# Performance work log

Hardware: AMD Instinct MI355X
Metric: run time of the kernel (lower is better)

## Reference

```python
import jax, jax.numpy as jnp
import numpy as np

B, S, D, H, R, P = 4, 8192, 512, 8, 64, 4
HD = D // H  # 64
EPS = 1e-6


def _sketch_p4(z, G1, G2):
    # sketchwithnegativity(z, 2): M1 = M2 = z
    inv_sqrt_r = 1.0 / np.sqrt(R).astype(np.float32)
    half = inv_sqrt_r * ((z @ G1) * (z @ G2))  # [B,H,S,R]
    return half * half  # sketch(): half * half for p=4


def setup_inputs() -> dict:
    key = jax.random.key(0)
    ks = jax.random.split(key, 16)
    lin = lambda k: jax.random.normal(k, (D, D), jnp.float32) * (1.0 / np.sqrt(D))
    g = lambda k: jax.random.normal(k, (HD, R), jnp.float32) * (1.0 / np.sqrt(R))
    return {
        "x": jax.random.normal(ks[0], (B, S, D), jnp.float32),
        "Wq": lin(ks[1]), "bq": jnp.zeros((D,), jnp.float32),
        "Wk": lin(ks[2]), "bk": jnp.zeros((D,), jnp.float32),
        "Wv": lin(ks[3]), "bv": jnp.zeros((D,), jnp.float32),
        "Wp": lin(ks[4]), "bp": jnp.zeros((D,), jnp.float32),
        "gamma_q": jnp.ones((1,), jnp.float32), "beta_q": jnp.zeros((1,), jnp.float32),
        "gamma_k": jnp.ones((1,), jnp.float32), "beta_k": jnp.zeros((1,), jnp.float32),
        "qG1": g(ks[5]), "qG2": g(ks[6]),
        "kG1": g(ks[7]), "kG2": g(ks[8]),
    }


def reference(x, Wq, bq, Wk, bk, Wv, bv, Wp, bp,
              gamma_q, beta_q, gamma_k, beta_k, qG1, qG2, kG1, kG2):
    b, s, d = x.shape
    split = lambda t: t.reshape(b, s, H, HD).transpose(0, 2, 1, 3)  # [B,H,S,HD]
    q = split(x @ Wq + bq)
    k = split(x @ Wk + bk)
    v = split(x @ Wv + bv)
    q = gamma_q * q + beta_q
    k = gamma_k * k + beta_k
    phi_q = _sketch_p4(q, qG1, qG2)  # [B,H,S,R]
    phi_k = _sketch_p4(k, kG1, kG2)  # [B,H,S,R]
    # linear-attention form of attn = (phi_q phi_k^T) / rowsum; avoids [S,S]
    kv = jnp.einsum('bhsr,bhsd->bhrd', phi_k, v)          # [B,H,R,HD]
    ksum = phi_k.sum(axis=2)                              # [B,H,R]
    num = jnp.einsum('bhqr,bhrd->bhqd', phi_q, kv)        # [B,H,S,HD]
    den = jnp.einsum('bhqr,bhr->bhq', phi_q, ksum) + EPS  # [B,H,S]
    out = num / den[..., None]
    out = out.transpose(0, 2, 1, 3).reshape(b, s, d)
    return out @ Wp + bp
```

## Files before the change

### kernel.cpp

```cpp
#include <hip/hip_runtime.h>
#include <hip/hip_bf16.h>


#define SEQ 8192

typedef __attribute__((ext_vector_type(8))) short bf16x8;
typedef __attribute__((ext_vector_type(4))) float f32x4;

__device__ __forceinline__ unsigned short f2b(float f) {
    union { float f; unsigned int i; } v; v.f = f;
    unsigned int r = v.i + 0x7fffu + ((v.i >> 16) & 1u);
    return (unsigned short)(r >> 16);
}
__device__ __forceinline__ float b2f(unsigned short u) {
    union { unsigned int i; float f; } v; v.i = ((unsigned int)u) << 16; return v.f;
}

#if __has_builtin(__builtin_amdgcn_global_load_lds)
#define ASYNC_CP 1
#endif

__device__ __forceinline__ void cp16(const unsigned short* g, unsigned short* l) {
#ifdef ASYNC_CP
    __builtin_amdgcn_global_load_lds(
        (const __attribute__((address_space(1))) unsigned int*)g,
        (__attribute__((address_space(3))) unsigned int*)l, 16, 0, 0);
#endif
}

#define SBAR      asm volatile("s_barrier" ::: "memory")
#define WAITV(n)  asm volatile("s_waitcnt vmcnt(" #n ")" ::: "memory")

__global__ __launch_bounds__(256) void prep_all(
    const float* __restrict__ x, unsigned short* __restrict__ xb,
    const float* __restrict__ Wv, const float* __restrict__ Wp,
    unsigned short* __restrict__ WTf, unsigned short* __restrict__ WTp,
    const float* __restrict__ Wq, const float* __restrict__ bq,
    const float* __restrict__ Wk, const float* __restrict__ bk,
    const float* __restrict__ bv,
    const float* __restrict__ gq, const float* __restrict__ bbq,
    const float* __restrict__ gk, const float* __restrict__ bbk,
    const float* __restrict__ qG1, const float* __restrict__ qG2,
    const float* __restrict__ kG1, const float* __restrict__ kG2,
    float* __restrict__ cvec)
{
    const int blk = blockIdx.x;
    const int tid = threadIdx.x;

    if (blk < 8192) {
        size_t i = ((size_t)blk * 256 + tid) * 8;
        float4 a = *(const float4*)&x[i];
        float4 b = *(const float4*)&x[i + 4];
        ushort4 o1 = { f2b(a.x), f2b(a.y), f2b(a.z), f2b(a.w) };
        ushort4 o2 = { f2b(b.x), f2b(b.y), f2b(b.z), f2b(b.w) };
        *(ushort4*)&xb[i]     = o1;
        *(ushort4*)&xb[i + 4] = o2;
        return;
    }

    if (blk < 8704) {
        const int idx = blk - 8192;
        const int z = idx >> 8;
        const float* W = (z == 0) ? Wv : Wp;
        unsigned short* O = (z == 0) ? (WTf + (size_t)2048 * 512) : WTp;
        __shared__ float t[32][33];
        const int tx = tid & 31, ty = tid >> 5;
        const int k0 = ((idx >> 4) & 15) * 32, n0 = (idx & 15) * 32;
        #pragma unroll
        for (int i = 0; i < 4; ++i)
            t[ty + 8 * i][tx] = W[(size_t)(k0 + ty + 8 * i) * 512 + n0 + tx];
        __syncthreads();
        #pragma unroll
        for (int i = 0; i < 4; ++i)
            O[(size_t)(n0 + ty + 8 * i) * 512 + k0 + tx] = f2b(t[tx][ty + 8 * i]);
        return;
    }

    const int idx = blk - 8704;
    if (idx == 512) {
        for (int i = tid; i < 512; i += 256) cvec[2048 + i] = bv[i];
        return;
    }
    const int bi = idx & 31, ky = idx >> 5;
    const int zz = bi >> 4, h = (bi >> 1) & 7, p = bi & 1;
    const float* W    = zz ? Wk : Wq;
    const float* bias = zz ? bk : bq;
    const float* G    = zz ? (p ? kG2 : kG1) : (p ? qG2 : qG1);
    const float  gamma = zz ? gk[0] : gq[0];
    const float  beta  = zz ? bbk[0] : bbq[0];

    __shared__ float Gs[64][65];
    for (int i = tid; i < 4096; i += 256) Gs[i >> 6][i & 63] = G[i];
    __syncthreads();

    const int rr = tid & 63, kg = tid >> 6;
    const int jc = zz * 1024 + h * 128 + rr * 2 + p;
    const int k0 = ky * 32;
    for (int k = k0 + kg; k < k0 + 32; k += 4) {
        float s = 0.f;
        const float* wrow = &W[(size_t)k * 512 + h * 64];
        #pragma unroll 8
        for (int j = 0; j < 64; ++j) s = fmaf(wrow[j], Gs[j][rr], s);
        WTf[(size_t)jc * 512 + k] = f2b(gamma * s);
    }
    if (kg == 0 && ky == 0) {
        float cb = 0.f, cg = 0.f;
        #pragma unroll 8
        for (int j = 0; j < 64; ++j) {
            cb = fmaf(bias[h * 64 + j], Gs[j][rr], cb);
            cg += Gs[j][rr];
        }
        cvec[jc] = gamma * cb + beta * cg;
    }
}

#define STAGE_P(kk, off)                                                        \
    do {                                                                        \
        unsigned short* dA = sm + (off) + (w * 32) * 32;                        \
        cp16(gA + (kk), dA);                                                    \
        cp16(gA + 16 * 512 + (kk), dA + 16 * 32);                               \
        unsigned short* dB = sm + (off) + 4096 + (w * 32) * 32;                 \
        cp16(gB + (kk), dB);                                                    \
        cp16(gB + 16 * 512 + (kk), dB + 16 * 32);                               \
    } while (0)

#define COMPUTE_P(off)                                                          \
    do {                                                                        \
        bf16x8 af[4], bfr[4];                                                   \
        _Pragma("unroll")                                                       \
        for (int i = 0; i < 4; ++i) {                                           \
            af[i]  = *(const bf16x8*)&sm[(off) + (wr * 64 + i * 16 + (lane & 15)) * 32 + cr]; \
            bfr[i] = *(const bf16x8*)&sm[(off) + 4096 + (wc * 64 + i * 16 + (lane & 15)) * 32 + cr]; \
        }                                                                       \
        __builtin_amdgcn_s_setprio(1);                                          \
        _Pragma("unroll")                                                       \
        for (int mi = 0; mi < 4; ++mi)                                          \
            _Pragma("unroll")                                                   \
            for (int ni = 0; ni < 4; ++ni)                                      \
                acc[mi][ni] = __builtin_amdgcn_mfma_f32_16x16x32_bf16(          \
                    af[mi], bfr[ni], acc[mi][ni], 0, 0, 0);                     \
        __builtin_amdgcn_s_setprio(0);                                          \
    } while (0)

#define KLOOP_P                                                                 \
    do {                                                                        \
        STAGE_P(0, 0u);                                                         \
        STAGE_P(32, 8192u);                                                     \
        unsigned o0 = 0u, o1 = 8192u, o2 = 16384u;                              \
        _Pragma("unroll 1")                                                     \
        for (int t = 0; t < 16; ++t) {                                          \
            SBAR;                               \
            if (t < 14) {                                                       \
                STAGE_P((t + 2) * 32, o2);                                      \
                WAITV(8);                       \
            } else if (t == 14) {                                               \
                WAITV(4);                                                       \
            } else {                                                            \
                WAITV(0);                                                       \
            }                                                                   \
            SBAR;                               \
            COMPUTE_P(o0);                                                      \
            unsigned tmp = o0; o0 = o1; o1 = o2; o2 = tmp;                      \
        }                                                                       \
    } while (0)

__global__ __launch_bounds__(256) void gemm_mfma_fused(
    const unsigned short* __restrict__ xb,
    const unsigned short* __restrict__ WTf,
    const float* __restrict__ cvec,
    unsigned short* __restrict__ PHIQ, unsigned short* __restrict__ PHIKT,
    unsigned short* __restrict__ VT)
{
    __shared__ __align__(16) unsigned short smem[24576];
    unsigned short* sm = smem;

    const int tid = threadIdx.x;
    const int w = tid >> 6, lane = tid & 63;
    const int flat = blockIdx.x;
    const int xcd = flat & 7, slot = flat >> 3;
    const int n0 = (xcd * 32 + slot / 20) * 128;
    const int j0 = (slot % 20) * 128;
    const int wr = w >> 1, wc = w & 1;

    const int r0 = w * 32 + (lane >> 2);
    const int kq = (lane & 3) * 8;
    const unsigned short* gA = &xb[(size_t)(n0 + r0) * 512 + kq];
    const unsigned short* gB = &WTf[(size_t)(j0 + r0) * 512 + kq];

    f32x4 acc[4][4];
    #pragma unroll
    for (int i = 0; i < 4; ++i)
        #pragma unroll
        for (int j = 0; j < 4; ++j) { acc[i][j] = (f32x4){0.f, 0.f, 0.f, 0.f}; }

    const int cr = (lane >> 4) * 8;

    KLOOP_P;

    const int bq = n0 >> 13;
    const int sq = n0 & (SEQ - 1);
    const int t0 = sq + wr * 64 + (lane >> 4) * 4;

    if (j0 < 2048) {
        const int zq = j0 >> 10;
        const int h  = (j0 >> 7) & 7;
        #pragma unroll
        for (int ni = 0; ni < 4; ++ni) {
            const int loc = wc * 64 + ni * 16 + (lane & 15);
            const float cv = cvec[j0 + loc];
            const int rr = loc >> 1;
            #pragma unroll
            for (int mi = 0; mi < 4; ++mi) {
                float ph[4];
                #pragma unroll
                for (int r = 0; r < 4; ++r) {
                    float u = acc[mi][ni][r] + cv;
                    float up = __shfl_xor(u, 1);
                    float hh = 0.125f * u * up;
                    ph[r] = hh * hh;
                }
                if ((lane & 1) == 0) {
                    if (zq == 0) {
                        #pragma unroll
                        for (int r = 0; r < 4; ++r)
                            PHIQ[((size_t)(bq * 8 + h) * SEQ + t0 + mi * 16 + r) * 64 + rr]
                                = f2b(ph[r]);
                    } else {
                        ushort4 o = { f2b(ph[0]), f2b(ph[1]), f2b(ph[2]), f2b(ph[3]) };
                        *(ushort4*)&PHIKT[((size_t)((bq * 8 + h) * 64 + rr)) * SEQ
                                          + t0 + mi * 16] = o;
                    }
                }
            }
        }
    } else {
        #pragma unroll
        for (int ni = 0; ni < 4; ++ni) {
            const int loc = wc * 64 + ni * 16 + (lane & 15);
            const int n = (j0 - 2048) + loc;
            const float cv = cvec[j0 + loc];
            #pragma unroll
            for (int mi = 0; mi < 4; ++mi) {
                ushort4 o = { f2b(acc[mi][ni][0] + cv), f2b(acc[mi][ni][1] + cv),
                              f2b(acc[mi][ni][2] + cv), f2b(acc[mi][ni][3] + cv) };
                *(ushort4*)&VT[((size_t)(bq * 512 + n)) * SEQ + t0 + mi * 16] = o;
            }
        }
    }
}

__global__ __launch_bounds__(256) void gemm_mfma_final(
    const unsigned short* __restrict__ Ab,
    const unsigned short* __restrict__ WTp,
    const float* __restrict__ bias, float* __restrict__ out)
{
    __shared__ __align__(16) unsigned short smem[24576];
    unsigned short* sm = smem;

    const int tid = threadIdx.x;
    const int w = tid >> 6, lane = tid & 63;
    const int flat = blockIdx.x;
    const int xcd = flat & 7, slot = flat >> 3;
    const int n0 = (xcd * 32 + (slot >> 2)) * 128;
    const int j0 = (slot & 3) * 128;
    const int wr = w >> 1, wc = w & 1;

    const int r0 = w * 32 + (lane >> 2);
    const int kq = (lane & 3) * 8;
    const unsigned short* gA = &Ab[(size_t)(n0 + r0) * 512 + kq];
    const unsigned short* gB = &WTp[(size_t)(j0 + r0) * 512 + kq];

    f32x4 acc[4][4];
    #pragma unroll
    for (int i = 0; i < 4; ++i)
        #pragma unroll
        for (int j = 0; j < 4; ++j) { acc[i][j] = (f32x4){0.f, 0.f, 0.f, 0.f}; }

    const int cr = (lane >> 4) * 8;

    KLOOP_P;

    #pragma unroll
    for (int ni = 0; ni < 4; ++ni) {
        const int jcol = j0 + wc * 64 + ni * 16 + (lane & 15);
        const float bvv = bias[jcol];
        #pragma unroll
        for (int mi = 0; mi < 4; ++mi) {
            #pragma unroll
            for (int r = 0; r < 4; ++r) {
                const int t = n0 + wr * 64 + mi * 16 + (lane >> 4) * 4 + r;
                out[(size_t)t * 512 + jcol] = acc[mi][ni][r] + bvv;
            }
        }
    }
}

__global__ __launch_bounds__(256) void kv_mfma(
    const unsigned short* __restrict__ PHIKT, const unsigned short* __restrict__ VT,
    float* __restrict__ KVP, float* __restrict__ KSP)
{
    const int bh = blockIdx.x, seg = blockIdx.y;
    const int tid = threadIdx.x;
    const int w = tid >> 6, lane = tid & 63;
    const size_t pbase =
        ((size_t)bh * 64 + w * 16 + (lane & 15)) * SEQ + seg * 256 + (lane >> 4) * 8;
    const size_t vbase =
        ((size_t)((bh >> 3) * 512 + (bh & 7) * 64 + (lane & 15))) * SEQ
        + seg * 256 + (lane >> 4) * 8;

    f32x4 acc[4], ks;
    #pragma unroll
    for (int nt = 0; nt < 4; ++nt) acc[nt] = (f32x4){0.f, 0.f, 0.f, 0.f};
    ks = (f32x4){0.f, 0.f, 0.f, 0.f};
    bf16x8 ones;
    #pragma unroll
    for (int i = 0; i < 8; ++i) ones[i] = (short)0x3f80;

    #pragma unroll 2
    for (int k = 0; k < 256; k += 32) {
        bf16x8 a = *(const bf16x8*)&PHIKT[pbase + k];
        ks = __builtin_amdgcn_mfma_f32_16x16x32_bf16(a, ones, ks, 0, 0, 0);
        #pragma unroll
        for (int nt = 0; nt < 4; ++nt) {
            bf16x8 bb = *(const bf16x8*)&VT[vbase + (size_t)nt * 16 * SEQ + k];
            acc[nt] = __builtin_amdgcn_mfma_f32_16x16x32_bf16(a, bb, acc[nt], 0, 0, 0);
        }
    }

    float* kvp = &KVP[((size_t)bh * 32 + seg) * 4096];
    #pragma unroll
    for (int nt = 0; nt < 4; ++nt) {
        float4 o = { acc[nt][0], acc[nt][1], acc[nt][2], acc[nt][3] };
        *(float4*)&kvp[(nt * 16 + (lane & 15)) * 64 + w * 16 + (lane >> 4) * 4] = o;
    }
    if ((lane & 15) == 0) {
        float4 o = { ks[0], ks[1], ks[2], ks[3] };
        *(float4*)&KSP[((size_t)bh * 32 + seg) * 64 + w * 16 + (lane >> 4) * 4] = o;
    }
}

__global__ __launch_bounds__(256) void kv_reduce(
    const float* __restrict__ KVP, const float* __restrict__ KSP,
    float* __restrict__ KV, float* __restrict__ KS)
{
    const int bh = blockIdx.x;
    const int e0 = blockIdx.y * 512;
    for (int e = e0 + threadIdx.x; e < e0 + 512; e += 256) {
        float s = 0.f;
        #pragma unroll 8
        for (int c = 0; c < 32; ++c) s += KVP[(size_t)(bh * 32 + c) * 4096 + e];
        KV[(size_t)bh * 4096 + e] = s;
    }
    if (blockIdx.y == 0 && threadIdx.x < 64) {
        float s = 0.f;
        for (int c = 0; c < 32; ++c) s += KSP[(bh * 32 + c) * 64 + threadIdx.x];
        KS[bh * 64 + threadIdx.x] = s;
    }
}

__global__ __launch_bounds__(256) void attn_mfma(
    const unsigned short* __restrict__ PHIQ, const float* __restrict__ KV,
    const float* __restrict__ KS, unsigned short* __restrict__ OAb)
{
    __shared__ __align__(16) unsigned short bpad[144 * 72];
    const int bh = blockIdx.x, st = blockIdx.y;
    const int tid = threadIdx.x;
    const int b = bh >> 3, h = bh & 7;

    for (int i = tid; i < 144 * 64; i += 256) {
        const int n = i >> 6, r = i & 63;
        float val;
        if (n < 64)        val = KV[(size_t)bh * 4096 + n * 64 + r];
        else if (n < 128)  { float x = KV[(size_t)bh * 4096 + (n - 64) * 64 + r];
                             val = x - b2f(f2b(x)); }
        else if (n == 128) val = KS[bh * 64 + r];
        else if (n == 129) { float x = KS[bh * 64 + r]; val = x - b2f(f2b(x)); }
        else               val = 0.f;
        bpad[n * 72 + r] = f2b(val);
    }
    __syncthreads();

    const int w = tid >> 6, lane = tid & 63;
    bf16x8 bf[9][2];
    #pragma unroll
    for (int nt = 0; nt < 9; ++nt) {
        const unsigned short* bp = &bpad[(nt * 16 + (lane & 15)) * 72 + (lane >> 4) * 8];
        bf[nt][0] = *(const bf16x8*)bp;
        bf[nt][1] = *(const bf16x8*)(bp + 32);
    }

    const int tw = st * 256 + w * 64;
    #pragma unroll
    for (int mt = 0; mt < 4; ++mt) {
        const unsigned short* ap =
            &PHIQ[((size_t)bh * SEQ + tw + mt * 16 + (lane & 15)) * 64 + (lane >> 4) * 8];
        bf16x8 a0 = *(const bf16x8*)ap;
        bf16x8 a1 = *(const bf16x8*)(ap + 32);
        f32x4 acc[9];
        #pragma unroll
        for (int nt = 0; nt < 9; ++nt) acc[nt] = (f32x4){0.f, 0.f, 0.f, 0.f};
        #pragma unroll
        for (int nt = 0; nt < 9; ++nt) {
            acc[nt] = __builtin_amdgcn_mfma_f32_16x16x32_bf16(a0, bf[nt][0], acc[nt], 0, 0, 0);
            acc[nt] = __builtin_amdgcn_mfma_f32_16x16x32_bf16(a1, bf[nt][1], acc[nt], 0, 0, 0);
        }
        #pragma unroll
        for (int r4 = 0; r4 < 4; ++r4) {
            const float den = __shfl(acc[8][r4], (lane & 48)) +
                              __shfl(acc[8][r4], (lane & 48) + 1) + 1e-6f;
            const float inv = 1.0f / den;
            const int s = tw + mt * 16 + (lane >> 4) * 4 + r4;
            #pragma unroll
            for (int nt = 0; nt < 4; ++nt)
                OAb[((size_t)b * SEQ + s) * 512 + h * 64 + nt * 16 + (lane & 15)] =
                    f2b((acc[nt][r4] + acc[nt + 4][r4]) * inv);
        }
    }
}

extern "C" void kernel_launch(void* const* d_in, const int* in_sizes, int n_in,
                              void* d_out, int out_size, void* d_ws, size_t ws_size,
                              hipStream_t stream)
{
    (void)in_sizes; (void)n_in; (void)out_size; (void)ws_size;
    const float* x   = (const float*)d_in[0];
    const float* Wq  = (const float*)d_in[1];
    const float* bq  = (const float*)d_in[2];
    const float* Wk  = (const float*)d_in[3];
    const float* bk  = (const float*)d_in[4];
    const float* Wv  = (const float*)d_in[5];
    const float* bv  = (const float*)d_in[6];
    const float* Wp  = (const float*)d_in[7];
    const float* bp  = (const float*)d_in[8];
    const float* gq  = (const float*)d_in[9];
    const float* bbq = (const float*)d_in[10];
    const float* gk  = (const float*)d_in[11];
    const float* bbk = (const float*)d_in[12];
    const float* qG1 = (const float*)d_in[13];
    const float* qG2 = (const float*)d_in[14];
    const float* kG1 = (const float*)d_in[15];
    const float* kG2 = (const float*)d_in[16];

    unsigned short* PHIQ  = (unsigned short*)d_ws;
    unsigned short* PHIKT = PHIQ + 16777216;
    unsigned short* VT    = PHIKT + 16777216;
    unsigned short* xb    = VT   + 16777216;
    unsigned short* OAb   = xb   + 16777216;
    unsigned short* WTf   = OAb  + 16777216;
    unsigned short* WTp   = WTf  + 2560 * 512;
    float* cvec = (float*)(WTp + 262144);
    float* KVP  = cvec + 2560;
    float* KSP  = KVP + 4194304;
    float* KV   = KSP + 65536;
    float* KS   = KV + 131072;
    float* out  = (float*)d_out;

    hipLaunchKernelGGL(prep_all, dim3(9217), dim3(256), 0, stream,
                       x, xb, Wv, Wp, WTf, WTp,
                       Wq, bq, Wk, bk, bv, gq, bbq, gk, bbk,
                       qG1, qG2, kG1, kG2, cvec);
    hipLaunchKernelGGL(gemm_mfma_fused, dim3(5120), dim3(256), 0, stream,
                       xb, WTf, cvec, PHIQ, PHIKT, VT);
    hipLaunchKernelGGL(kv_mfma, dim3(32, 32), dim3(256), 0, stream,
                       PHIKT, VT, KVP, KSP);
    hipLaunchKernelGGL(kv_reduce, dim3(32, 8), dim3(256), 0, stream, KVP, KSP, KV, KS);
    hipLaunchKernelGGL(attn_mfma, dim3(32, 32), dim3(256), 0, stream,
                       PHIQ, KV, KS, OAb);
    hipLaunchKernelGGL(gemm_mfma_final, dim3(1024), dim3(256), 0, stream,
                       OAb, WTp, bp, out);
}
```

Baseline: 390.0 us.

## Widen fused projection GEMM tile to 128x256 with double-buffered pipeline

Doubles the N-dimension tile of the fused QKV/sketch GEMM from 128 to 256 columns, so each wave computes a 64x128 sub-tile with 32 accumulators and the grid halves to 2560 blocks. The k-loop changes from a triple-buffered to a double-buffered LDS pipeline to fit the larger B tile in the same 24576-element shared buffer. This raises arithmetic intensity and cuts redundant reloads of the x tile, at the cost of more accumulator registers (possible lower occupancy) and a shallower prefetch depth.

```diff
diff --git a/kernel.cpp b/kernel.cpp
--- a/kernel.cpp
+++ b/kernel.cpp
@@ -114,54 +114,35 @@
     }
 }
 
-#define STAGE_P(kk, off)                                                        \
+#define STAGE_W(kk, off)                                                        \
     do {                                                                        \
         unsigned short* dA = sm + (off) + (w * 32) * 32;                        \
         cp16(gA + (kk), dA);                                                    \
         cp16(gA + 16 * 512 + (kk), dA + 16 * 32);                               \
-        unsigned short* dB = sm + (off) + 4096 + (w * 32) * 32;                 \
+        unsigned short* dB = sm + (off) + 4096 + (w * 64) * 32;                 \
         cp16(gB + (kk), dB);                                                    \
         cp16(gB + 16 * 512 + (kk), dB + 16 * 32);                               \
+        cp16(gB + 32 * 512 + (kk), dB + 32 * 32);                               \
+        cp16(gB + 48 * 512 + (kk), dB + 48 * 32);                               \
     } while (0)
 
-#define COMPUTE_P(off)                                                          \
+#define COMPUTE_W(off)                                                          \
     do {                                                                        \
-        bf16x8 af[4], bfr[4];                                                   \
+        bf16x8 af[4], bfr[8];                                                   \
         _Pragma("unroll")                                                       \
-        for (int i = 0; i < 4; ++i) {                                           \
-            af[i]  = *(const bf16x8*)&sm[(off) + (wr * 64 + i * 16 + (lane & 15)) * 32 + cr]; \
-            bfr[i] = *(const bf16x8*)&sm[(off) + 4096 + (wc * 64 + i * 16 + (lane & 15)) * 32 + cr]; \
-        }                                                                       \
+        for (int i = 0; i < 4; ++i)                                             \
+            af[i] = *(const bf16x8*)&sm[(off) + (wr * 64 + i * 16 + (lane & 15)) * 32 + cr]; \
+        _Pragma("unroll")                                                       \
+        for (int i = 0; i < 8; ++i)                                             \
+            bfr[i] = *(const bf16x8*)&sm[(off) + 4096 + (wc * 128 + i * 16 + (lane & 15)) * 32 + cr]; \
         __builtin_amdgcn_s_setprio(1);                                          \
         _Pragma("unroll")                                                       \
         for (int mi = 0; mi < 4; ++mi)                                          \
             _Pragma("unroll")                                                   \
-            for (int ni = 0; ni < 4; ++ni)                                      \
+            for (int ni = 0; ni < 8; ++ni)                                      \
                 acc[mi][ni] = __builtin_amdgcn_mfma_f32_16x16x32_bf16(          \
                     af[mi], bfr[ni], acc[mi][ni], 0, 0, 0);                     \
         __builtin_amdgcn_s_setprio(0);                                          \
-    } while (0)
-
-#define KLOOP_P                                                                 \
-    do {                                                                        \
-        STAGE_P(0, 0u);                                                         \
-        STAGE_P(32, 8192u);                                                     \
-        unsigned o0 = 0u, o1 = 8192u, o2 = 16384u;                              \
-        _Pragma("unroll 1")                                                     \
-        for (int t = 0; t < 16; ++t) {                                          \
-            SBAR;                               \
-            if (t < 14) {                                                       \
-                STAGE_P((t + 2) * 32, o2);                                      \
-                WAITV(8);                       \
-            } else if (t == 14) {                                               \
-                WAITV(4);                                                       \
-            } else {                                                            \
-                WAITV(0);                                                       \
-            }                                                                   \
-            SBAR;                               \
-            COMPUTE_P(o0);                                                      \
-            unsigned tmp = o0; o0 = o1; o1 = o2; o2 = tmp;                      \
-        }                                                                       \
     } while (0)
 
 __global__ __launch_bounds__(256) void gemm_mfma_fused(
@@ -178,24 +159,37 @@
     const int w = tid >> 6, lane = tid & 63;
     const int flat = blockIdx.x;
     const int xcd = flat & 7, slot = flat >> 3;
-    const int n0 = (xcd * 32 + slot / 20) * 128;
-    const int j0 = (slot % 20) * 128;
+    const int n0 = (xcd * 32 + slot / 10) * 128;
+    const int j0 = (slot % 10) * 256;
     const int wr = w >> 1, wc = w & 1;
 
-    const int r0 = w * 32 + (lane >> 2);
+    const int r0a = w * 32 + (lane >> 2);
+    const int r0b = w * 64 + (lane >> 2);
     const int kq = (lane & 3) * 8;
-    const unsigned short* gA = &xb[(size_t)(n0 + r0) * 512 + kq];
-    const unsigned short* gB = &WTf[(size_t)(j0 + r0) * 512 + kq];
-
-    f32x4 acc[4][4];
+    const unsigned short* gA = &xb[(size_t)(n0 + r0a) * 512 + kq];
+    const unsigned short* gB = &WTf[(size_t)(j0 + r0b) * 512 + kq];
+
+    f32x4 acc[4][8];
     #pragma unroll
     for (int i = 0; i < 4; ++i)
         #pragma unroll
-        for (int j = 0; j < 4; ++j) { acc[i][j] = (f32x4){0.f, 0.f, 0.f, 0.f}; }
+        for (int j = 0; j < 8; ++j) { acc[i][j] = (f32x4){0.f, 0.f, 0.f, 0.f}; }
 
     const int cr = (lane >> 4) * 8;
 
-    KLOOP_P;
+    STAGE_W(0, 0u);
+    #pragma unroll 1
+    for (int t = 0; t < 16; ++t) {
+        SBAR;
+        if (t + 1 < 16) {
+            STAGE_W((t + 1) * 32, (unsigned)(((t + 1) & 1) * 12288));
+            WAITV(6);
+        } else {
+            WAITV(0);
+        }
+        SBAR;
+        COMPUTE_W((unsigned)((t & 1) * 12288));
+    }
 
     const int bq = n0 >> 13;
     const int sq = n0 & (SEQ - 1);
@@ -203,12 +197,12 @@
 
     if (j0 < 2048) {
         const int zq = j0 >> 10;
-        const int h  = (j0 >> 7) & 7;
-        #pragma unroll
-        for (int ni = 0; ni < 4; ++ni) {
-            const int loc = wc * 64 + ni * 16 + (lane & 15);
+        #pragma unroll
+        for (int ni = 0; ni < 8; ++ni) {
+            const int loc = wc * 128 + ni * 16 + (lane & 15);
             const float cv = cvec[j0 + loc];
-            const int rr = loc >> 1;
+            const int h  = ((j0 + wc * 128 + ni * 16) >> 7) & 7;
+            const int rr = (ni * 16 + (lane & 15)) >> 1;
             #pragma unroll
             for (int mi = 0; mi < 4; ++mi) {
                 float ph[4];
@@ -235,8 +229,8 @@
         }
     } else {
         #pragma unroll
-        for (int ni = 0; ni < 4; ++ni) {
-            const int loc = wc * 64 + ni * 16 + (lane & 15);
+        for (int ni = 0; ni < 8; ++ni) {
+            const int loc = wc * 128 + ni * 16 + (lane & 15);
             const int n = (j0 - 2048) + loc;
             const float cv = cvec[j0 + loc];
             #pragma unroll
@@ -248,6 +242,56 @@
         }
     }
 }
+
+#define STAGE_P(kk, off)                                                        \
+    do {                                                                        \
+        unsigned short* dA = sm + (off) + (w * 32) * 32;                        \
+        cp16(gA + (kk), dA);                                                    \
+        cp16(gA + 16 * 512 + (kk), dA + 16 * 32);                               \
+        unsigned short* dB = sm + (off) + 4096 + (w * 32) * 32;                 \
+        cp16(gB + (kk), dB);                                                    \
+        cp16(gB + 16 * 512 + (kk), dB + 16 * 32);                               \
+    } while (0)
+
+#define COMPUTE_P(off)                                                          \
+    do {                                                                        \
+        bf16x8 af[4], bfr[4];                                                   \
+        _Pragma("unroll")                                                       \
+        for (int i = 0; i < 4; ++i) {                                           \
+            af[i]  = *(const bf16x8*)&sm[(off) + (wr * 64 + i * 16 + (lane & 15)) * 32 + cr]; \
+            bfr[i] = *(const bf16x8*)&sm[(off) + 4096 + (wc * 64 + i * 16 + (lane & 15)) * 32 + cr]; \
+        }                                                                       \
+        __builtin_amdgcn_s_setprio(1);                                          \
+        _Pragma("unroll")                                                       \
+        for (int mi = 0; mi < 4; ++mi)                                          \
+            _Pragma("unroll")                                                   \
+            for (int ni = 0; ni < 4; ++ni)                                      \
+                acc[mi][ni] = __builtin_amdgcn_mfma_f32_16x16x32_bf16(          \
+                    af[mi], bfr[ni], acc[mi][ni], 0, 0, 0);                     \
+        __builtin_amdgcn_s_setprio(0);                                          \
+    } while (0)
+
+#define KLOOP_P                                                                 \
+    do {                                                                        \
+        STAGE_P(0, 0u);                                                         \
+        STAGE_P(32, 8192u);                                                     \
+        unsigned o0 = 0u, o1 = 8192u, o2 = 16384u;                              \
+        _Pragma("unroll 1")                                                     \
+        for (int t = 0; t < 16; ++t) {                                          \
+            SBAR;                                                               \
+            if (t < 14) {                                                       \
+                STAGE_P((t + 2) * 32, o2);                                      \
+                WAITV(8);                                                       \
+            } else if (t == 14) {                                               \
+                WAITV(4);                                                       \
+            } else {                                                            \
+                WAITV(0);                                                       \
+            }                                                                   \
+            SBAR;                                                               \
+            COMPUTE_P(o0);                                                      \
+            unsigned tmp = o0; o0 = o1; o1 = o2; o2 = tmp;                      \
+        }                                                                       \
+    } while (0)
 
 __global__ __launch_bounds__(256) void gemm_mfma_final(
     const unsigned short* __restrict__ Ab,
@@ -459,7 +503,7 @@
                        x, xb, Wv, Wp, WTf, WTp,
                        Wq, bq, Wk, bk, bv, gq, bbq, gk, bbk,
                        qG1, qG2, kG1, kG2, cvec);
-    hipLaunchKernelGGL(gemm_mfma_fused, dim3(5120), dim3(256), 0, stream,
+    hipLaunchKernelGGL(gemm_mfma_fused, dim3(2560), dim3(256), 0, stream,
                        xb, WTf, cvec, PHIQ, PHIKT, VT);
     hipLaunchKernelGGL(kv_mfma, dim3(32, 32), dim3(256), 0, stream,
                        PHIKT, VT, KVP, KSP);
```

Result: slower. 428.6 us (+9.9%).

## Load GEMM MFMA fragments directly from global into registers, dropping LDS staging

Applied to the files above, without the earlier changes.

Both projection GEMM kernels stop staging tiles through LDS with async global-to-LDS copies and barriers. Each wave now loads its bf16 A/B fragments straight from global memory into registers, double-buffering them in registers and interleaving loads with MFMA blocks. This removes barrier synchronization and the LDS footprint. In exchange, blocks lose sharing of tiles across waves, so global and L2 traffic rises (each A row is read by two waves), and the small 16-byte per-lane loads are strided across rows.

```diff
diff --git a/kernel.cpp b/kernel.cpp
--- a/kernel.cpp
+++ b/kernel.cpp
@@ -15,21 +15,6 @@
 __device__ __forceinline__ float b2f(unsigned short u) {
     union { unsigned int i; float f; } v; v.i = ((unsigned int)u) << 16; return v.f;
 }
-
-#if __has_builtin(__builtin_amdgcn_global_load_lds)
-#define ASYNC_CP 1
-#endif
-
-__device__ __forceinline__ void cp16(const unsigned short* g, unsigned short* l) {
-#ifdef ASYNC_CP
-    __builtin_amdgcn_global_load_lds(
-        (const __attribute__((address_space(1))) unsigned int*)g,
-        (__attribute__((address_space(3))) unsigned int*)l, 16, 0, 0);
-#endif
-}
-
-#define SBAR      asm volatile("s_barrier" ::: "memory")
-#define WAITV(n)  asm volatile("s_waitcnt vmcnt(" #n ")" ::: "memory")
 
 __global__ __launch_bounds__(256) void prep_all(
     const float* __restrict__ x, unsigned short* __restrict__ xb,
@@ -114,53 +99,37 @@
     }
 }
 
-#define STAGE_P(kk, off)                                                        \
+#define LOADF(AF, BF, kk)                                                       \
     do {                                                                        \
-        unsigned short* dA = sm + (off) + (w * 32) * 32;                        \
-        cp16(gA + (kk), dA);                                                    \
-        cp16(gA + 16 * 512 + (kk), dA + 16 * 32);                               \
-        unsigned short* dB = sm + (off) + 4096 + (w * 32) * 32;                 \
-        cp16(gB + (kk), dB);                                                    \
-        cp16(gB + 16 * 512 + (kk), dB + 16 * 32);                               \
-    } while (0)
-
-#define COMPUTE_P(off)                                                          \
-    do {                                                                        \
-        bf16x8 af[4], bfr[4];                                                   \
         _Pragma("unroll")                                                       \
         for (int i = 0; i < 4; ++i) {                                           \
-            af[i]  = *(const bf16x8*)&sm[(off) + (wr * 64 + i * 16 + (lane & 15)) * 32 + cr]; \
-            bfr[i] = *(const bf16x8*)&sm[(off) + 4096 + (wc * 64 + i * 16 + (lane & 15)) * 32 + cr]; \
+            AF[i] = *(const bf16x8*)(pA[i] + (kk));                             \
+            BF[i] = *(const bf16x8*)(pB[i] + (kk));                             \
         }                                                                       \
+    } while (0)
+
+#define MFMA16(AF, BF)                                                          \
+    do {                                                                        \
         __builtin_amdgcn_s_setprio(1);                                          \
         _Pragma("unroll")                                                       \
         for (int mi = 0; mi < 4; ++mi)                                          \
             _Pragma("unroll")                                                   \
             for (int ni = 0; ni < 4; ++ni)                                      \
                 acc[mi][ni] = __builtin_amdgcn_mfma_f32_16x16x32_bf16(          \
-                    af[mi], bfr[ni], acc[mi][ni], 0, 0, 0);                     \
+                    AF[mi], BF[ni], acc[mi][ni], 0, 0, 0);                      \
         __builtin_amdgcn_s_setprio(0);                                          \
     } while (0)
 
-#define KLOOP_P                                                                 \
+#define KLOOP_REG                                                               \
     do {                                                                        \
-        STAGE_P(0, 0u);                                                         \
-        STAGE_P(32, 8192u);                                                     \
-        unsigned o0 = 0u, o1 = 8192u, o2 = 16384u;                              \
-        _Pragma("unroll 1")                                                     \
-        for (int t = 0; t < 16; ++t) {                                          \
-            SBAR;                               \
-            if (t < 14) {                                                       \
-                STAGE_P((t + 2) * 32, o2);                                      \
-                WAITV(8);                       \
-            } else if (t == 14) {                                               \
-                WAITV(4);                                                       \
-            } else {                                                            \
-                WAITV(0);                                                       \
-            }                                                                   \
-            SBAR;                               \
-            COMPUTE_P(o0);                                                      \
-            unsigned tmp = o0; o0 = o1; o1 = o2; o2 = tmp;                      \
+        bf16x8 aX[4], bX[4], aY[4], bY[4];                                      \
+        LOADF(aX, bX, 0);                                                       \
+        _Pragma("unroll")                                                       \
+        for (int t = 0; t < 16; t += 2) {                                       \
+            if (t + 1 < 16) LOADF(aY, bY, (t + 1) * 32);                        \
+            MFMA16(aX, bX);                                                     \
+            if (t + 2 < 16) LOADF(aX, bX, (t + 2) * 32);                        \
+            MFMA16(aY, bY);                                                     \
         }                                                                       \
     } while (0)
 
@@ -171,9 +140,6 @@
     unsigned short* __restrict__ PHIQ, unsigned short* __restrict__ PHIKT,
     unsigned short* __restrict__ VT)
 {
-    __shared__ __align__(16) unsigned short smem[24576];
-    unsigned short* sm = smem;
-
     const int tid = threadIdx.x;
     const int w = tid >> 6, lane = tid & 63;
     const int flat = blockIdx.x;
@@ -182,10 +148,16 @@
     const int j0 = (slot % 20) * 128;
     const int wr = w >> 1, wc = w & 1;
 
-    const int r0 = w * 32 + (lane >> 2);
-    const int kq = (lane & 3) * 8;
-    const unsigned short* gA = &xb[(size_t)(n0 + r0) * 512 + kq];
-    const unsigned short* gB = &WTf[(size_t)(j0 + r0) * 512 + kq];
+    const int rm = lane & 15;
+    const int kq = (lane >> 4) * 8;
+
+    const unsigned short* pA[4];
+    const unsigned short* pB[4];
+    #pragma unroll
+    for (int i = 0; i < 4; ++i) {
+        pA[i] = &xb [(size_t)(n0 + wr * 64 + i * 16 + rm) * 512 + kq];
+        pB[i] = &WTf[(size_t)(j0 + wc * 64 + i * 16 + rm) * 512 + kq];
+    }
 
     f32x4 acc[4][4];
     #pragma unroll
@@ -193,9 +165,7 @@
         #pragma unroll
         for (int j = 0; j < 4; ++j) { acc[i][j] = (f32x4){0.f, 0.f, 0.f, 0.f}; }
 
-    const int cr = (lane >> 4) * 8;
-
-    KLOOP_P;
+    KLOOP_REG;
 
     const int bq = n0 >> 13;
     const int sq = n0 & (SEQ - 1);
@@ -254,9 +224,6 @@
     const unsigned short* __restrict__ WTp,
     const float* __restrict__ bias, float* __restrict__ out)
 {
-    __shared__ __align__(16) unsigned short smem[24576];
-    unsigned short* sm = smem;
-
     const int tid = threadIdx.x;
     const int w = tid >> 6, lane = tid & 63;
     const int flat = blockIdx.x;
@@ -265,10 +232,16 @@
     const int j0 = (slot & 3) * 128;
     const int wr = w >> 1, wc = w & 1;
 
-    const int r0 = w * 32 + (lane >> 2);
-    const int kq = (lane & 3) * 8;
-    const unsigned short* gA = &Ab[(size_t)(n0 + r0) * 512 + kq];
-    const unsigned short* gB = &WTp[(size_t)(j0 + r0) * 512 + kq];
+    const int rm = lane & 15;
+    const int kq = (lane >> 4) * 8;
+
+    const unsigned short* pA[4];
+    const unsigned short* pB[4];
+    #pragma unroll
+    for (int i = 0; i < 4; ++i) {
+        pA[i] = &Ab [(size_t)(n0 + wr * 64 + i * 16 + rm) * 512 + kq];
+        pB[i] = &WTp[(size_t)(j0 + wc * 64 + i * 16 + rm) * 512 + kq];
+    }
 
     f32x4 acc[4][4];
     #pragma unroll
@@ -276,9 +249,7 @@
         #pragma unroll
         for (int j = 0; j < 4; ++j) { acc[i][j] = (f32x4){0.f, 0.f, 0.f, 0.f}; }
 
-    const int cr = (lane >> 4) * 8;
-
-    KLOOP_P;
+    KLOOP_REG;
 
     #pragma unroll
     for (int ni = 0; ni < 4; ++ni) {
```

Measured after the change: 601.0 us. 1.54x slower.
